# Kernel tuning notes

Hardware: AMD Instinct MI355X
Metric: run time of the kernel (lower is better)

## Reference

```python
import jax, jax.numpy as jnp
import numpy as np

B, S, D, H = 2, 2048, 1024, 16
DK = D // H  # 64
THETA = 10000.0
SCALE = 1.0 / np.sqrt(DK)


def _rope(t, pos):
    """Apply rotary embedding. t: [b,h,s,dk], pos: [b,s] int."""
    inv_freq = THETA ** (-jnp.arange(0, DK, 2, dtype=jnp.float32) / DK)  # [dk/2]
    ang = pos[:, None, :, None].astype(jnp.float32) * inv_freq  # [b,1,s,dk/2]
    cos, sin = jnp.cos(ang), jnp.sin(ang)
    t1, t2 = t[..., 0::2], t[..., 1::2]  # interleaved pairs
    rot = jnp.stack([t1 * cos - t2 * sin, t1 * sin + t2 * cos], axis=-1)
    return rot.reshape(t.shape)


def setup_inputs() -> dict:
    key = jax.random.key(0)
    ks = jax.random.split(key, 9)
    sc = 0.02
    x = jax.random.normal(ks[0], (B, S, D), jnp.float32)
    token_position = jnp.tile(jnp.arange(S, dtype=jnp.int32)[None, :], (B, 1))
    Wq = jax.random.normal(ks[1], (D, D), jnp.float32) * sc
    Wk = jax.random.normal(ks[2], (D, D), jnp.float32) * sc
    Wv = jax.random.normal(ks[3], (D, D), jnp.float32) * sc
    Wo = jax.random.normal(ks[4], (D, D), jnp.float32) * sc
    bq = jnp.zeros((D,), jnp.float32)
    bk = jnp.zeros((D,), jnp.float32)
    bv = jnp.zeros((D,), jnp.float32)
    bo = jnp.zeros((D,), jnp.float32)
    return {"x": x, "token_position": token_position,
            "Wq": Wq, "bq": bq, "Wk": Wk, "bk": bk,
            "Wv": Wv, "bv": bv, "Wo": Wo, "bo": bo}


def reference(x, token_position, Wq, bq, Wk, bk, Wv, bv, Wo, bo):
    b, s, d = x.shape
    # projections, split heads: [b,s,d] -> [b,h,s,dk]
    def heads(t):
        return t.reshape(b, s, H, DK).transpose(0, 2, 1, 3)
    q = heads(x @ Wq + bq)
    k = heads(x @ Wk + bk)
    v = heads(x @ Wv + bv)
    q = _rope(q, token_position)
    k = _rope(k, token_position)
    scores = jnp.einsum('bhnk,bhmk->bhnm', q, k) * SCALE  # [b,h,s,s]
    causal = jnp.tril(jnp.ones((s, s), dtype=bool))
    scores = jnp.where(causal, scores, -jnp.inf)
    probs = jax.nn.softmax(scores, axis=-1)
    o = jnp.einsum('bhnm,bhmk->bhnk', probs, v)  # [b,h,s,dk]
    o = o.transpose(0, 2, 1, 3).reshape(b, s, d)
    return o @ Wo + bo
```

## Files before the change

kernel.cpp:

```cpp
#include <hip/hip_runtime.h>
#include <math.h>

#define BB  2
#define SS  2048
#define DD  1024
#define HH  16
#define DKK 64

constexpr float kScale = 0.125f;
constexpr float kC1 = 0.18033688011112042f;
constexpr float kC2 = 23.0831206542234144f;

typedef __bf16 bf16x8 __attribute__((ext_vector_type(8)));
typedef float f32x4 __attribute__((ext_vector_type(4)));

__device__ __forceinline__ void async_copy16(const void* g, void* l) {
  __builtin_amdgcn_global_load_lds(
      (const __attribute__((address_space(1))) void*)g,
      (__attribute__((address_space(3))) void*)l, 16, 0, 0);
}

__global__ __launch_bounds__(256) void prep_kernel(
    const float* __restrict__ x, const int* __restrict__ pos,
    const float* __restrict__ W0, const float* __restrict__ W1,
    const float* __restrict__ W2, const float* __restrict__ W3,
    __bf16* __restrict__ xb, float2* __restrict__ rtab,
    __bf16* __restrict__ T0, __bf16* __restrict__ T1,
    __bf16* __restrict__ T2, __bf16* __restrict__ T3) {
  __shared__ __bf16 tile[64][65];
  const int bid = blockIdx.x;
  const int t = threadIdx.x;
  if (bid < 2048) {
    const size_t i = ((size_t)bid * 256 + t) * 8;
    const float4 v0 = *(const float4*)(x + i);
    const float4 v1 = *(const float4*)(x + i + 4);
    bf16x8 o;
    o[0] = (__bf16)v0.x; o[1] = (__bf16)v0.y; o[2] = (__bf16)v0.z; o[3] = (__bf16)v0.w;
    o[4] = (__bf16)v1.x; o[5] = (__bf16)v1.y; o[6] = (__bf16)v1.z; o[7] = (__bf16)v1.w;
    *(bf16x8*)(xb + i) = o;
  } else if (bid < 2560) {
    const int idx = (bid - 2048) * 256 + t;
    const int m = idx >> 5, pi = idx & 31;
    const float inv = exp2f(-0.4152410118609203f * (float)pi);
    float sn, cs;
    __sincosf((float)pos[m] * inv, &sn, &cs);
    rtab[idx] = make_float2(cs, sn);
  } else {
    const int tid2 = bid - 2560;
    const int z = tid2 >> 8, rem = tid2 & 255;
    const float* W;
    __bf16* T;
    switch (z) {
      case 0: W = W0; T = T0; break;
      case 1: W = W1; T = T1; break;
      case 2: W = W2; T = T2; break;
      default: W = W3; T = T3; break;
    }
    const int k0 = (rem >> 4) * 64, n0 = (rem & 15) * 64;
    const int c = t & 63, rg = t >> 6;
#pragma unroll
    for (int i = 0; i < 16; i++) {
      const int r = rg + i * 4;
      tile[r][c] = (__bf16)W[(size_t)(k0 + r) * DD + n0 + c];
    }
    __syncthreads();
#pragma unroll
    for (int i = 0; i < 16; i++) {
      const int r = rg + i * 4;
      T[(size_t)(n0 + r) * DD + k0 + c] = tile[c][r];
    }
  }
}

__device__ __forceinline__ void gemm_core(
    const __bf16* __restrict__ A, const __bf16* __restrict__ Bt,
    int bm, int bn, f32x4 (&acc)[4][4], __bf16* As, __bf16* Bs) {
  const int t = threadIdx.x;
  const int lane = t & 63, wave = t >> 6;
  const int col = lane & 15, quad = lane >> 4;
  const int wm = (wave & 1) * 64, wn = (wave >> 1) * 64;
  const int r8 = lane >> 3;
  const int cg = (lane & 7) ^ r8;
  const __bf16* ag = A + (size_t)(bm + wave * 32 + r8) * DD + cg * 8;
  const __bf16* bg = Bt + (size_t)(bn + wave * 32 + r8) * DD + cg * 8;
  __bf16* asb = As + wave * 32 * 64;
  __bf16* bsb = Bs + wave * 32 * 64;

  for (int kt = 0; kt < DD; kt += 64) {
#pragma unroll
    for (int c = 0; c < 4; c++) {
      async_copy16(ag + (size_t)c * 8 * DD + kt, asb + c * 512);
      async_copy16(bg + (size_t)c * 8 * DD + kt, bsb + c * 512);
    }
    __syncthreads();
#pragma unroll
    for (int ks = 0; ks < 2; ks++) {
      bf16x8 af[4], bf[4];
#pragma unroll
      for (int i = 0; i < 4; i++)
        af[i] = *(const bf16x8*)(As + (wm + i * 16 + col) * 64 +
                                 (((ks * 4 + quad) ^ (col & 7)) * 8));
#pragma unroll
      for (int j = 0; j < 4; j++)
        bf[j] = *(const bf16x8*)(Bs + (wn + j * 16 + col) * 64 +
                                 (((ks * 4 + quad) ^ (col & 7)) * 8));
#pragma unroll
      for (int i = 0; i < 4; i++)
#pragma unroll
        for (int j = 0; j < 4; j++)
          acc[i][j] =
              __builtin_amdgcn_mfma_f32_16x16x32_bf16(af[i], bf[j], acc[i][j], 0, 0, 0);
    }
    __syncthreads();
  }
}

__global__ __launch_bounds__(256) void qkv_gemm_kernel(
    const __bf16* __restrict__ xb, const __bf16* __restrict__ WqT,
    const __bf16* __restrict__ WkT, const __bf16* __restrict__ WvT,
    const float* __restrict__ bq, const float* __restrict__ bk,
    const float* __restrict__ bv, const float2* __restrict__ ropetab,
    __bf16* __restrict__ qo, __bf16* __restrict__ ko, __bf16* __restrict__ vo) {
  __shared__ __bf16 As[128 * 64];
  __shared__ __bf16 Bs[128 * 64];
  const int mat = blockIdx.x >> 3;
  const int bn = (blockIdx.x & 7) * 128;
  const int bm = blockIdx.y * 128;

  f32x4 acc[4][4] = {};
  const int t = threadIdx.x, lane = t & 63, wave = t >> 6;
  const int col = lane & 15, quad = lane >> 4;
  const int wm = (wave & 1) * 64, wn = (wave >> 1) * 64;

  if (mat == 2) {
    gemm_core(WvT, xb, bn, bm, acc, As, Bs);
    const int b = bm >> 11;
#pragma unroll
    for (int i = 0; i < 4; i++) {
#pragma unroll
      for (int r = 0; r < 4; r++) {
        const int n = bn + wm + i * 16 + quad * 4 + r;
        const float bb = bv[n];
        const int h = n >> 6, dk = n & 63;
        __bf16* vrow = vo + ((size_t)(b * HH + h) * DKK + dk) * SS;
#pragma unroll
        for (int j = 0; j < 4; j++) {
          const int m = bm + wn + j * 16 + col;
          vrow[m & (SS - 1)] = (__bf16)(acc[i][j][r] + bb);
        }
      }
    }
    return;
  }

  const __bf16* Bt = mat == 0 ? WqT : WkT;
  const float* bias = mat == 0 ? bq : bk;
  __bf16* out = mat == 0 ? qo : ko;
  gemm_core(xb, Bt, bm, bn, acc, As, Bs);

#pragma unroll
  for (int i = 0; i < 4; i++) {
#pragma unroll
    for (int j = 0; j < 4; j++) {
      const int n = bn + wn + j * 16 + col;
      const float bb = bias[n];
      const int pi = (n & 63) >> 1;
#pragma unroll
      for (int r = 0; r < 4; r++) {
        const int m = bm + wm + i * 16 + quad * 4 + r;
        float v = acc[i][j][r] + bb;
        {
          const float other = __shfl_xor(v, 1, 64);
          const float2 cssn = ropetab[(size_t)m * 32 + pi];
          v = (n & 1) ? (other * cssn.y + v * cssn.x)
                      : (v * cssn.x - other * cssn.y);
        }
        const int h = n >> 6, dk = n & 63;
        const int b = m >> 11, s = m & (SS - 1);
        out[((size_t)(b * HH + h) * SS + s) * DKK + dk] = (__bf16)v;
      }
    }
  }
}

__global__ __launch_bounds__(256) void oproj_gemm_kernel(
    const __bf16* __restrict__ ob, const __bf16* __restrict__ WoT,
    const float* __restrict__ bo, float* __restrict__ out) {
  __shared__ __bf16 As[128 * 64];
  __shared__ __bf16 Bs[128 * 64];
  const int bn = blockIdx.x * 128;
  const int bm = blockIdx.y * 128;
  f32x4 acc[4][4] = {};
  gemm_core(ob, WoT, bm, bn, acc, As, Bs);

  const int t = threadIdx.x, lane = t & 63, wave = t >> 6;
  const int col = lane & 15, quad = lane >> 4;
  const int wm = (wave & 1) * 64, wn = (wave >> 1) * 64;
#pragma unroll
  for (int i = 0; i < 4; i++) {
#pragma unroll
    for (int j = 0; j < 4; j++) {
      const int n = bn + wn + j * 16 + col;
      const float bb = bo[n];
#pragma unroll
      for (int r = 0; r < 4; r++) {
        const int m = bm + wm + i * 16 + quad * 4 + r;
        out[(size_t)m * DD + n] = acc[i][j][r] + bb;
      }
    }
  }
}

__global__ __launch_bounds__(256) void flash_attn_mfma_kernel(
    const __bf16* __restrict__ q, const __bf16* __restrict__ k,
    const __bf16* __restrict__ vt, __bf16* __restrict__ o) {
  __shared__ __bf16 Ks[64 * 64];
  __shared__ __bf16 Vs[64 * 64];
  __shared__ __bf16 Ps[4][16 * 72];

  const int bh = blockIdx.x;
  const int pr = blockIdx.y;
  const int t = threadIdx.x, lane = t & 63, wave = t >> 6;
  const int col = lane & 15, quad = lane >> 4;
  const int r8 = lane >> 3;
  const int cg = (lane & 7) ^ r8;

  const __bf16* qb = q + (size_t)bh * SS * DKK;
  const __bf16* kb = k + (size_t)bh * SS * DKK;
  const __bf16* vtb = vt + (size_t)bh * DKK * SS;
  const int b = bh / HH, h = bh % HH;
  __bf16* pw = (__bf16*)Ps[wave];

#pragma unroll
  for (int phase = 0; phase < 2; phase++) {
    const int qt = phase == 0 ? pr : (31 - pr);
    const int rbase = qt * 64 + wave * 16;

    bf16x8 qf[2];
#pragma unroll
    for (int ks = 0; ks < 2; ks++)
      qf[ks] = *(const bf16x8*)(qb + (size_t)(rbase + col) * DKK + ks * 32 +
                                quad * 8);

    f32x4 oacc[4] = {};
    float l_lane[4] = {0.f, 0.f, 0.f, 0.f};

    for (int kt = 0; kt <= qt; kt++) {
#pragma unroll
      for (int i = 0; i < 2; i++) {
        const int slab = wave * 2 + i;
        async_copy16(kb + (size_t)(kt * 64 + slab * 8 + r8) * DKK + cg * 8,
                     Ks + slab * 512);
        async_copy16(vtb + (size_t)(slab * 8 + r8) * SS + kt * 64 + cg * 8,
                     Vs + slab * 512);
      }
      __syncthreads();

      f32x4 sc[4] = {};
#pragma unroll
      for (int ct = 0; ct < 4; ct++)
#pragma unroll
        for (int ks = 0; ks < 2; ks++) {
          const bf16x8 kf = *(const bf16x8*)(Ks + (ct * 16 + col) * 64 +
                                             (((ks * 4 + quad) ^ (col & 7)) * 8));
          sc[ct] = __builtin_amdgcn_mfma_f32_16x16x32_bf16(qf[ks], kf, sc[ct],
                                                           0, 0, 0);
        }

      const bool diag = (kt == qt);
#pragma unroll
      for (int ct = 0; ct < 4; ct++)
#pragma unroll
        for (int r = 0; r < 4; r++) {
          float p = exp2f(sc[ct][r] * kC1 - kC2);
          if (diag && (kt * 64 + ct * 16 + col) > (rbase + quad * 4 + r))
            p = 0.0f;
          l_lane[r] += p;
          pw[(quad * 4 + r) * 72 + ct * 16 + col] = (__bf16)p;
        }

      {
        bf16x8 pf[2];
#pragma unroll
        for (int ks = 0; ks < 2; ks++)
          pf[ks] = *(const bf16x8*)(pw + col * 72 + ks * 32 + quad * 8);
#pragma unroll
        for (int dt = 0; dt < 4; dt++)
#pragma unroll
          for (int ks = 0; ks < 2; ks++) {
            const bf16x8 vf = *(const bf16x8*)(Vs + (dt * 16 + col) * 64 +
                                               (((ks * 4 + quad) ^ (col & 7)) * 8));
            oacc[dt] = __builtin_amdgcn_mfma_f32_16x16x32_bf16(pf[ks], vf,
                                                               oacc[dt], 0, 0, 0);
          }
      }
      __syncthreads();
    }

#pragma unroll
    for (int r = 0; r < 4; r++) {
      float l = l_lane[r];
#pragma unroll
      for (int w = 1; w < 16; w <<= 1) l += __shfl_xor(l, w, 64);
      const float inv_l = 1.0f / l;
      const int s = rbase + quad * 4 + r;
#pragma unroll
      for (int dt = 0; dt < 4; dt++)
        o[((size_t)(b * SS + s) * HH + h) * DKK + dt * 16 + col] =
            (__bf16)(oacc[dt][r] * inv_l);
    }
  }
}

extern "C" void kernel_launch(void* const* d_in, const int* in_sizes, int n_in,
                              void* d_out, int out_size, void* d_ws,
                              size_t ws_size, hipStream_t stream) {
  const float* x  = (const float*)d_in[0];
  const int*  pos = (const int*)d_in[1];
  const float* Wq = (const float*)d_in[2];
  const float* bq = (const float*)d_in[3];
  const float* Wk = (const float*)d_in[4];
  const float* bk = (const float*)d_in[5];
  const float* Wv = (const float*)d_in[6];
  const float* bv = (const float*)d_in[7];
  const float* Wo = (const float*)d_in[8];
  const float* bo = (const float*)d_in[9];
  float* out = (float*)d_out;

  char* ws = (char*)d_ws;
  __bf16* xb  = (__bf16*)(ws);
  __bf16* WqT = (__bf16*)(ws + ((size_t)8  << 20));
  __bf16* WkT = (__bf16*)(ws + ((size_t)10 << 20));
  __bf16* WvT = (__bf16*)(ws + ((size_t)12 << 20));
  __bf16* WoT = (__bf16*)(ws + ((size_t)14 << 20));
  __bf16* qb  = (__bf16*)(ws + ((size_t)16 << 20));
  __bf16* kb  = (__bf16*)(ws + ((size_t)24 << 20));
  __bf16* vtb = (__bf16*)(ws + ((size_t)32 << 20));
  __bf16* ob  = (__bf16*)(ws + ((size_t)40 << 20));
  float2* rtab = (float2*)(ws + ((size_t)48 << 20));

  prep_kernel<<<3584, 256, 0, stream>>>(x, pos, Wq, Wk, Wv, Wo, xb, rtab, WqT,
                                        WkT, WvT, WoT);
  qkv_gemm_kernel<<<dim3(24, 32), 256, 0, stream>>>(xb, WqT, WkT, WvT, bq, bk,
                                                    bv, rtab, qb, kb, vtb);
  flash_attn_mfma_kernel<<<dim3(32, 16), 256, 0, stream>>>(qb, kb, vtb, ob);
  oproj_gemm_kernel<<<dim3(8, 32), 256, 0, stream>>>(ob, WoT, bo, out);
}
```

Before: 206.0 us.

## Double-buffer K/V tiles and widen flash-attention query tile to 128 rows

The attention kernel now handles 128 query rows per block, 32 per wave, so each K/V tile loaded into LDS is reused by twice as many rows. The grid is halved to match. K/V tiles are double-buffered so the async load of the next tile overlaps compute on the current one, which removes one barrier per iteration. Masking is applied only on diagonal tiles and fully masked tiles are skipped. The QK product is computed transposed so P is written as packed 4-element stores. The cost is more registers and LDS per block and fewer blocks, which may lower occupancy.

Result: slower. 212.1 us (+2.9%).

```diff
diff --git a/kernel.cpp b/kernel.cpp
--- a/kernel.cpp
+++ b/kernel.cpp
@@ -12,6 +12,7 @@
 constexpr float kC2 = 23.0831206542234144f;
 
 typedef __bf16 bf16x8 __attribute__((ext_vector_type(8)));
+typedef __bf16 bf16x4 __attribute__((ext_vector_type(4)));
 typedef float f32x4 __attribute__((ext_vector_type(4)));
 
 __device__ __forceinline__ void async_copy16(const void* g, void* l) {
@@ -211,12 +212,71 @@
   }
 }
 
+template <bool kMask>
+__device__ __forceinline__ void attn_tile(
+    const __bf16* __restrict__ Kbuf, const __bf16* __restrict__ Vbuf,
+    __bf16* __restrict__ pw, const bf16x8 (&qf)[2][2], f32x4 (&oacc)[2][4],
+    float (&l_lane)[2], int tok0, int rbase_w, int col, int quad) {
+  bf16x8 kf[4][2];
+#pragma unroll
+  for (int ct = 0; ct < 4; ct++)
+#pragma unroll
+    for (int ks = 0; ks < 2; ks++)
+      kf[ct][ks] = *(const bf16x8*)(Kbuf + (ct * 16 + col) * 64 +
+                                    (((ks * 4 + quad) ^ (col & 7)) * 8));
+#pragma unroll
+  for (int rt = 0; rt < 2; rt++) {
+    f32x4 sc[4] = {};
+#pragma unroll
+    for (int ct = 0; ct < 4; ct++)
+#pragma unroll
+      for (int ks = 0; ks < 2; ks++)
+        sc[ct] = __builtin_amdgcn_mfma_f32_16x16x32_bf16(kf[ct][ks],
+                                                         qf[rt][ks], sc[ct],
+                                                         0, 0, 0);
+    const int rg = rbase_w + rt * 16 + col;
+#pragma unroll
+    for (int ct = 0; ct < 4; ct++) {
+      bf16x4 pk;
+#pragma unroll
+      for (int r = 0; r < 4; r++) {
+        float p = exp2f(sc[ct][r] * kC1 - kC2);
+        if (kMask && (tok0 + ct * 16 + quad * 4 + r) > rg) p = 0.0f;
+        l_lane[rt] += p;
+        pk[r] = (__bf16)p;
+      }
+      *(bf16x4*)(pw + (rt * 16 + col) * 72 + ct * 16 + quad * 4) = pk;
+    }
+  }
+  bf16x8 vf[4][2];
+#pragma unroll
+  for (int dt = 0; dt < 4; dt++)
+#pragma unroll
+    for (int ks = 0; ks < 2; ks++)
+      vf[dt][ks] = *(const bf16x8*)(Vbuf + (dt * 16 + col) * 64 +
+                                    (((ks * 4 + quad) ^ (col & 7)) * 8));
+#pragma unroll
+  for (int rt = 0; rt < 2; rt++) {
+    bf16x8 pf[2];
+#pragma unroll
+    for (int ks = 0; ks < 2; ks++)
+      pf[ks] =
+          *(const bf16x8*)(pw + (rt * 16 + col) * 72 + ks * 32 + quad * 8);
+#pragma unroll
+    for (int dt = 0; dt < 4; dt++)
+#pragma unroll
+      for (int ks = 0; ks < 2; ks++)
+        oacc[rt][dt] = __builtin_amdgcn_mfma_f32_16x16x32_bf16(
+            pf[ks], vf[dt][ks], oacc[rt][dt], 0, 0, 0);
+  }
+}
+
 __global__ __launch_bounds__(256) void flash_attn_mfma_kernel(
     const __bf16* __restrict__ q, const __bf16* __restrict__ k,
     const __bf16* __restrict__ vt, __bf16* __restrict__ o) {
-  __shared__ __bf16 Ks[64 * 64];
-  __shared__ __bf16 Vs[64 * 64];
-  __shared__ __bf16 Ps[4][16 * 72];
+  __shared__ __bf16 Ks[2][64 * 64];
+  __shared__ __bf16 Vs[2][64 * 64];
+  __shared__ __bf16 Ps[4][32 * 72];
 
   const int bh = blockIdx.x;
   const int pr = blockIdx.y;
@@ -233,81 +293,76 @@
 
 #pragma unroll
   for (int phase = 0; phase < 2; phase++) {
-    const int qt = phase == 0 ? pr : (31 - pr);
-    const int rbase = qt * 64 + wave * 16;
-
-    bf16x8 qf[2];
-#pragma unroll
-    for (int ks = 0; ks < 2; ks++)
-      qf[ks] = *(const bf16x8*)(qb + (size_t)(rbase + col) * DKK + ks * 32 +
-                                quad * 8);
-
-    f32x4 oacc[4] = {};
-    float l_lane[4] = {0.f, 0.f, 0.f, 0.f};
-
-    for (int kt = 0; kt <= qt; kt++) {
-#pragma unroll
-      for (int i = 0; i < 2; i++) {
-        const int slab = wave * 2 + i;
-        async_copy16(kb + (size_t)(kt * 64 + slab * 8 + r8) * DKK + cg * 8,
-                     Ks + slab * 512);
-        async_copy16(vtb + (size_t)(slab * 8 + r8) * SS + kt * 64 + cg * 8,
-                     Vs + slab * 512);
-      }
+    const int qt = phase == 0 ? pr : (15 - pr);
+    const int rbase_w = qt * 128 + wave * 32;
+
+    bf16x8 qf[2][2];
+#pragma unroll
+    for (int rt = 0; rt < 2; rt++)
+#pragma unroll
+      for (int ks = 0; ks < 2; ks++)
+        qf[rt][ks] = *(const bf16x8*)(qb +
+                                      (size_t)(rbase_w + rt * 16 + col) * DKK +
+                                      ks * 32 + quad * 8);
+
+    f32x4 oacc[2][4] = {};
+    float l_lane[2] = {0.f, 0.f};
+
+    const int nkt = 2 * qt + 2;
+
+#pragma unroll
+    for (int i = 0; i < 2; i++) {
+      const int slab = wave * 2 + i;
+      async_copy16(kb + (size_t)(slab * 8 + r8) * DKK + cg * 8,
+                   Ks[0] + slab * 512);
+      async_copy16(vtb + (size_t)(slab * 8 + r8) * SS + cg * 8,
+                   Vs[0] + slab * 512);
+    }
+
+    for (int kt = 0; kt < nkt; kt++) {
+      const int cur = kt & 1;
       __syncthreads();
 
-      f32x4 sc[4] = {};
-#pragma unroll
-      for (int ct = 0; ct < 4; ct++)
-#pragma unroll
-        for (int ks = 0; ks < 2; ks++) {
-          const bf16x8 kf = *(const bf16x8*)(Ks + (ct * 16 + col) * 64 +
-                                             (((ks * 4 + quad) ^ (col & 7)) * 8));
-          sc[ct] = __builtin_amdgcn_mfma_f32_16x16x32_bf16(qf[ks], kf, sc[ct],
-                                                           0, 0, 0);
+      if (kt + 1 < nkt) {
+#pragma unroll
+        for (int i = 0; i < 2; i++) {
+          const int slab = wave * 2 + i;
+          async_copy16(
+              kb + (size_t)((kt + 1) * 64 + slab * 8 + r8) * DKK + cg * 8,
+              Ks[cur ^ 1] + slab * 512);
+          async_copy16(
+              vtb + (size_t)(slab * 8 + r8) * SS + (kt + 1) * 64 + cg * 8,
+              Vs[cur ^ 1] + slab * 512);
         }
-
-      const bool diag = (kt == qt);
-#pragma unroll
-      for (int ct = 0; ct < 4; ct++)
-#pragma unroll
-        for (int r = 0; r < 4; r++) {
-          float p = exp2f(sc[ct][r] * kC1 - kC2);
-          if (diag && (kt * 64 + ct * 16 + col) > (rbase + quad * 4 + r))
-            p = 0.0f;
-          l_lane[r] += p;
-          pw[(quad * 4 + r) * 72 + ct * 16 + col] = (__bf16)p;
-        }
-
-      {
-        bf16x8 pf[2];
-#pragma unroll
-        for (int ks = 0; ks < 2; ks++)
-          pf[ks] = *(const bf16x8*)(pw + col * 72 + ks * 32 + quad * 8);
+      }
+
+      const int tok0 = kt * 64;
+      if (tok0 <= rbase_w + 31) {
+        if (tok0 + 63 <= rbase_w)
+          attn_tile<false>(Ks[cur], Vs[cur], pw, qf, oacc, l_lane, tok0,
+                           rbase_w, col, quad);
+        else
+          attn_tile<true>(Ks[cur], Vs[cur], pw, qf, oacc, l_lane, tok0,
+                          rbase_w, col, quad);
+      }
+    }
+    __syncthreads();
+
+#pragma unroll
+    for (int rt = 0; rt < 2; rt++) {
+      float l = l_lane[rt];
+      l += __shfl_xor(l, 16, 64);
+      l += __shfl_xor(l, 32, 64);
+#pragma unroll
+      for (int r = 0; r < 4; r++) {
+        const float lr = __shfl(l, quad * 4 + r, 64);
+        const float inv_l = 1.0f / lr;
+        const int s = rbase_w + rt * 16 + quad * 4 + r;
 #pragma unroll
         for (int dt = 0; dt < 4; dt++)
-#pragma unroll
-          for (int ks = 0; ks < 2; ks++) {
-            const bf16x8 vf = *(const bf16x8*)(Vs + (dt * 16 + col) * 64 +
-                                               (((ks * 4 + quad) ^ (col & 7)) * 8));
-            oacc[dt] = __builtin_amdgcn_mfma_f32_16x16x32_bf16(pf[ks], vf,
-                                                               oacc[dt], 0, 0, 0);
-          }
-      }
-      __syncthreads();
-    }
-
-#pragma unroll
-    for (int r = 0; r < 4; r++) {
-      float l = l_lane[r];
-#pragma unroll
-      for (int w = 1; w < 16; w <<= 1) l += __shfl_xor(l, w, 64);
-      const float inv_l = 1.0f / l;
-      const int s = rbase + quad * 4 + r;
-#pragma unroll
-      for (int dt = 0; dt < 4; dt++)
-        o[((size_t)(b * SS + s) * HH + h) * DKK + dt * 16 + col] =
-            (__bf16)(oacc[dt][r] * inv_l);
+          o[((size_t)(b * SS + s) * HH + h) * DKK + dt * 16 + col] =
+              (__bf16)(oacc[rt][dt][r] * inv_l);
+      }
     }
   }
 }
@@ -343,6 +398,6 @@
                                         WkT, WvT, WoT);
   qkv_gemm_kernel<<<dim3(24, 32), 256, 0, stream>>>(xb, WqT, WkT, WvT, bq, bk,
                                                     bv, rtab, qb, kb, vtb);
-  flash_attn_mfma_kernel<<<dim3(32, 16), 256, 0, stream>>>(qb, kb, vtb, ob);
+  flash_attn_mfma_kernel<<<dim3(32, 8), 256, 0, stream>>>(qb, kb, vtb, ob);
   oproj_gemm_kernel<<<dim3(8, 32), 256, 0, stream>>>(ob, WoT, bo, out);
 }
```
